# Performance work log

Hardware: AMD Instinct MI355X
Metric: run time of the kernel (lower is better)

Reference implementation:

```python
import jax, jax.numpy as jnp
import numpy as np
from jax import lax

BN_EPS = 1e-5
SP_NEAR = 2


def fps(xyz, m):
    # xyz: [b, n, c] -> indices [b, m]; deterministic start at index 0
    b, n, _ = xyz.shape
    def step(carry, _):
        dist, far = carry
        centroid = jnp.take_along_axis(xyz, far[:, None, None], axis=1)  # [b,1,c]
        d = jnp.sum((xyz - centroid) ** 2, axis=-1)                      # [b,n]
        dist = jnp.minimum(dist, d)
        return (dist, jnp.argmax(dist, axis=-1).astype(jnp.int32)), far
    init = (jnp.full((b, n), jnp.inf, xyz.dtype), jnp.zeros((b,), jnp.int32))
    _, idxs = lax.scan(step, init, None, length=m)
    return jnp.transpose(idxs)  # [b, m]


def knn(x, k):
    # x: [b, n, c] -> k nearest (incl. self) indices [b, n, k]
    sq = jnp.sum(x * x, axis=-1)
    d = sq[:, :, None] + sq[:, None, :] - 2.0 * jnp.einsum('bnc,bmc->bnm', x, x)
    return lax.top_k(-d, k)[1]


def gather_cf(x, idx):
    # channel-first index_points: x [b, c, n], idx [b, ...] -> [b, c, *idx.shape[1:]]
    b, c = x.shape[:2]
    flat = idx.reshape(b, -1)
    g = jnp.take_along_axis(x, flat[:, None, :], axis=2)
    return g.reshape((b, c) + idx.shape[1:])


def gather_cl(x, idx):
    # channel-last index_points: x [b, n, c], idx [b, ...] -> [b, *idx.shape[1:], c]
    b, c = x.shape[0], x.shape[-1]
    flat = idx.reshape(b, -1)
    g = jnp.take_along_axis(x, flat[:, :, None], axis=1)
    return g.reshape((b,) + idx.shape[1:] + (c,))


def bn_act(x, gamma, beta, nd):
    # inference-mode BatchNorm (running mean 0, var 1) + exact GELU; Dropout is identity in eval
    shp = (1, -1) + (1,) * nd
    scale = 1.0 / jnp.sqrt(1.0 + BN_EPS)
    return jax.nn.gelu(gamma.reshape(shp) * (x * scale) + beta.reshape(shp), approximate=False)


def setup_inputs() -> dict:
    key = jax.random.key(0)
    ks = jax.random.split(key, 8)
    BS, SP_IN, SP_OUT, DN_IN, DN_OUT = 128, 256, 256, 128, 128
    N_STK, N_STK_PNT, COOR = 32, 32, 32
    return {
        'sparse_fea': jax.random.normal(ks[0], (BS, SP_IN, N_STK), jnp.float32),
        'dense_fea': jax.random.normal(ks[1], (BS, DN_IN, N_STK, N_STK_PNT), jnp.float32),
        'stk_coor': jax.random.normal(ks[2], (BS, N_STK, COOR), jnp.float32),
        'n_stk_center': 16,
        'sp_w': jax.random.normal(ks[3], (SP_OUT, 2 * SP_IN), jnp.float32) * 0.02,
        'sp_b': jnp.zeros((SP_OUT,), jnp.float32),
        'sp_g': jnp.ones((SP_OUT,), jnp.float32),
        'sp_beta': jnp.zeros((SP_OUT,), jnp.float32),
        'dn_w': jax.random.normal(ks[4], (DN_OUT, 2 * DN_IN), jnp.float32) * 0.02,
        'dn_b': jnp.zeros((DN_OUT,), jnp.float32),
        'dn_g': jnp.ones((DN_OUT,), jnp.float32),
        'dn_beta': jnp.zeros((DN_OUT,), jnp.float32),
        'ds_w': jax.random.normal(ks[5], (DN_OUT, DN_IN, 1, 3), jnp.float32) * 0.05,
        'ds_b': jnp.zeros((DN_OUT,), jnp.float32),
        'ds_g': jnp.ones((DN_OUT,), jnp.float32),
        'ds_beta': jnp.zeros((DN_OUT,), jnp.float32),
    }


def reference(sparse_fea, dense_fea, stk_coor, n_stk_center,
              sp_w, sp_b, sp_g, sp_beta,
              dn_w, dn_b, dn_g, dn_beta,
              ds_w, ds_b, ds_g, ds_beta):
    bs, dn_in, n_stk, n_stk_pnt = dense_fea.shape
    fps_idx = fps(stk_coor, n_stk_center)            # [b, m]
    # --- sparse branch ---
    sc = gather_cf(sparse_fea, fps_idx)              # [b, c, m]
    knn_all = knn(stk_coor, SP_NEAR)                 # [b, n, k]
    knn_fps = gather_cl(knn_all, fps_idx)            # [b, m, k]
    sn = gather_cf(sparse_fea, knn_fps)              # [b, c, m, k]
    sa = sn - sc[:, :, :, None]
    sp_x = jnp.concatenate([sa, jnp.broadcast_to(sc[:, :, :, None], sa.shape)], axis=1)  # [b,2c,m,k]
    sp_x = jnp.einsum('bimk,oi->bomk', sp_x, sp_w) + sp_b[None, :, None, None]
    sp_x = bn_act(sp_x, sp_g, sp_beta, 2)
    sparse_out = jnp.max(sp_x, axis=3)               # [b, sp_out, m]
    # --- dense branch ---
    # 'b c s sp -> b s (sp c)'
    d_flat = jnp.transpose(dense_fea, (0, 2, 3, 1)).reshape(bs, n_stk, n_stk_pnt * dn_in)
    dc = gather_cl(d_flat, fps_idx)                  # [b, m, sp*c]
    dnb = gather_cl(d_flat, knn_fps)                 # [b, m, k, sp*c]
    da = dnb - dc[:, :, None, :]
    dcat = jnp.concatenate([da, jnp.broadcast_to(dc[:, :, None, :], da.shape)], axis=3)  # [b,m,k,2*sp*c]
    # 'b s n (sp c) -> b c s sp n' with sp=n_stk_pnt (exact torch reshape semantics)
    d5 = dcat.reshape(bs, fps_idx.shape[1], SP_NEAR, n_stk_pnt, 2 * dn_in)
    d5 = jnp.transpose(d5, (0, 4, 1, 3, 2))          # [b, 2c, m, sp, k]
    d5 = jnp.einsum('bimpn,oi->bompn', d5, dn_w) + dn_b[None, :, None, None, None]
    d5 = bn_act(d5, dn_g, dn_beta, 3)
    d4 = jnp.max(d5, axis=4)                         # [b, dn_out, m, sp]
    y = lax.conv_general_dilated(d4, ds_w, window_strides=(1, 2), padding=((0, 0), (1, 1)),
                                 dimension_numbers=('NCHW', 'OIHW', 'NCHW')) + ds_b[None, :, None, None]
    dense_out = bn_act(y, ds_g, ds_beta, 2)          # [b, dn_out, m, sp//2]
    coor_out = gather_cl(stk_coor, fps_idx)          # [b, m, coor]
    return sparse_out, dense_out, coor_out
```

## Files before the change

### kernel.cpp

```cpp
#include <hip/hip_runtime.h>


typedef unsigned short u16;
typedef unsigned int   u32;
typedef __attribute__((ext_vector_type(8))) short bf16x8;
typedef __attribute__((ext_vector_type(4))) float f32x4;

#define BN_SCALE 0.9999950000374997f

__device__ __forceinline__ float gelu_f(float x){
  return 0.5f*x*(1.0f + erff(x*0.70710678118654752f));
}
__device__ __forceinline__ u16 f2bf(float f){
  u32 x = __float_as_uint(f);
  x += 0x7fffu + ((x>>16)&1u);
  return (u16)(x>>16);
}

__global__ __launch_bounds__(256) void k_prep(
    const float* __restrict__ dn_w, const float* __restrict__ ds_w, const float* __restrict__ sp_w,
    const float* __restrict__ coor,
    u16* __restrict__ wdb, u16* __restrict__ wcb, u16* __restrict__ wsb,
    int* __restrict__ fps_idx, int* __restrict__ nn_idx, float* __restrict__ coor_out)
{
  int blk = blockIdx.x, t = threadIdx.x;
  if (blk < 128){
    int w = blk*256 + t;
    int j=w&7, lane=(w>>3)&63, tile=w>>9;
    int kt=tile>>3, ot=tile&7;
    int o=ot*16+(lane&15), i=kt*32+((lane>>4)&3)*8+j;
    wdb[w] = f2bf(dn_w[o*256+i]);
  } else if (blk < 320){
    int w = (blk-128)*256 + t;
    int j=w&7, lane=(w>>3)&63, tile=w>>9;
    int kt=tile>>3, ot=tile&7;
    int o=ot*16+(lane&15), k=kt*32+((lane>>4)&3)*8+j;
    wcb[w] = f2bf(ds_w[o*384+k]);
  } else if (blk < 832){
    int w = (blk-320)*256 + t;
    int j=w&7, lane=(w>>3)&63, tile=w>>9;
    int kt=tile>>4, ot=tile&15;
    int o=ot*16+(lane&15), i=kt*32+((lane>>4)&3)*8+j;
    wsb[w] = f2bf(sp_w[o*512+i]);
  } else {
    int b = blk - 832;
    __shared__ float Xs[32*33];
    __shared__ float D[32*33];
    __shared__ int   s_sel[16];
    for (int i=t;i<1024;i+=256) Xs[(i>>5)*33 + (i&31)] = coor[b*1024+i];
    __syncthreads();
    #pragma unroll
    for (int k2=0;k2<4;k2++){
      int p=t+k2*256, i=p>>5, j=p&31;
      float d=0.f;
      #pragma unroll
      for (int c=0;c<32;c++){ float df=Xs[i*33+c]-Xs[j*33+c]; d+=df*df; }
      D[i*33+j]=d;
    }
    __syncthreads();
    if (t < 64){
      int j = t & 31;
      float dist = 3.0e38f;
      int far = 0;
      #pragma unroll
      for (int it=0; it<16; ++it){
        if (t==0) s_sel[it]=far;
        dist = fminf(dist, D[far*33+j]);
        float v=dist; int idx=j;
        #pragma unroll
        for (int off=16; off>=1; off>>=1){
          float v2=__shfl_xor(v,off,32); int i2=__shfl_xor(idx,off,32);
          if (v2>v || (v2==v && i2<idx)){ v=v2; idx=i2; }
        }
        far = idx;
      }
      if (t==0){
        #pragma unroll
        for (int it=0;it<16;++it) fps_idx[b*16+it]=s_sel[it];
      }
    }
    __syncthreads();
    {
      int wv=t>>6, j=t&31;
      #pragma unroll
      for (int q=0;q<4;q++){
        int it = wv*4+q, sel = s_sel[it];
        float d = D[sel*33+j];
        if (j==sel) d=3.0e38f;
        float v=d; int idx=j;
        #pragma unroll
        for (int off=16; off>=1; off>>=1){
          float v2=__shfl_xor(v,off,32); int i2=__shfl_xor(idx,off,32);
          if (v2<v || (v2==v && i2<idx)){ v=v2; idx=i2; }
        }
        if ((t&63)==0) nn_idx[b*16+it]=idx;
      }
    }
    for (int q=t;q<512;q+=256){
      int mm=q>>5, c=q&31;
      coor_out[b*512+q] = Xs[s_sel[mm]*33 + c];
    }
  }
}

__global__ __launch_bounds__(256) void k_main(
    const float* __restrict__ sfea, const u16* __restrict__ wsb,
    const float* __restrict__ sp_b, const float* __restrict__ sp_g, const float* __restrict__ sp_be,
    const float* __restrict__ dfea, const u16* __restrict__ wdb,
    const float* __restrict__ dn_b, const float* __restrict__ dn_g, const float* __restrict__ dn_be,
    const u16* __restrict__ wcb,
    const float* __restrict__ ds_b, const float* __restrict__ ds_g, const float* __restrict__ ds_be,
    const int* __restrict__ fps_idx, const int* __restrict__ nn_idx,
    float* __restrict__ out_sp, float* __restrict__ out_dn)
{
  __shared__ char smem[36352];
  __shared__ int SI[64];
  int blk=blockIdx.x;
  int t=threadIdx.x, lane=t&63, wv=t>>6, quad=lane>>4, col=lane&15;
  if (blk < 64){
    int b0 = blk*2;
    u16*   Xb = (u16*)smem;
    float* P  = (float*)(smem+33280);
    if (t<64){
      int bb=t>>5, q=t&31, b=b0+bb;
      SI[t] = ((q<16) ? fps_idx[b*16+q] : nn_idx[b*16+(q-16)]) & 31;
    }
    { float A = sp_g[t]*BN_SCALE; P[t]=A; P[256+t]=fmaf(sp_b[t],A,sp_be[t]); }
    __syncthreads();
    #pragma unroll
    for (int bb=0;bb<2;bb++){
      const float* row = sfea + (b0+bb)*8192 + t*32;
      #pragma unroll
      for (int m=0;m<16;m++){
        float vc=row[SI[bb*32+m]], vn=row[SI[bb*32+16+m]];
        Xb[bb*8320 + m*520 + t]       = f2bf(vn-vc);
        Xb[bb*8320 + m*520 + 256 + t] = f2bf(vc);
      }
    }
    __syncthreads();
    #pragma unroll
    for (int oh=0;oh<2;oh++){
      f32x4 accA[2][2]={}, accB[2][2]={};
      #pragma unroll
      for (int kt=0;kt<16;kt++){
        bf16x8 bf0 = *(const bf16x8*)&Xb[        col*520 + kt*32 + quad*8];
        bf16x8 bf1 = *(const bf16x8*)&Xb[8320 +  col*520 + kt*32 + quad*8];
        #pragma unroll
        for (int r=0;r<2;r++){
          bf16x8 afr = *(const bf16x8*)&wsb[((kt*16 + oh*8 + wv + r*4)*64+lane)*8];
          if (kt<8){
            accA[0][r]=__builtin_amdgcn_mfma_f32_16x16x32_bf16(afr,bf0,accA[0][r],0,0,0);
            accA[1][r]=__builtin_amdgcn_mfma_f32_16x16x32_bf16(afr,bf1,accA[1][r],0,0,0);
          } else {
            accB[0][r]=__builtin_amdgcn_mfma_f32_16x16x32_bf16(afr,bf0,accB[0][r],0,0,0);
            accB[1][r]=__builtin_amdgcn_mfma_f32_16x16x32_bf16(afr,bf1,accB[1][r],0,0,0);
          }
        }
      }
      #pragma unroll
      for (int bb=0;bb<2;bb++){
        #pragma unroll
        for (int r=0;r<2;r++){
          #pragma unroll
          for (int reg=0;reg<4;reg++){
            int o = oh*128 + (wv+r*4)*16 + quad*4 + reg;
            float A=P[o], Bv=P[256+o];
            float k1 = accA[bb][r][reg]+accB[bb][r][reg];
            float k0 = accB[bb][r][reg];
            float v = fmaxf(gelu_f(fmaf(k1,A,Bv)), gelu_f(fmaf(k0,A,Bv)));
            out_sp[((b0+bb)*256+o)*16 + col] = v;
          }
        }
      }
    }
  } else {
    int d=blk-64;
    int b = ((d>>6)<<3) | (d&7), m0 = ((d>>3)&7)*2;
    u16* Vb = (u16*)smem;
    u16* Bc = (u16*)smem;
    float* Pd = (float*)(smem+33792);
    if (t < 128){
      float A  = dn_g[t]*BN_SCALE; float Bv = fmaf(dn_b[t], A, dn_be[t]);
      float Ac = ds_g[t]*BN_SCALE; float Cv = fmaf(ds_b[t], Ac, ds_be[t]);
      Pd[t]=A; Pd[128+t]=Bv; Pd[256+t]=Ac; Pd[384+t]=Cv;
      Pd[512+t]=gelu_f(Bv);
    }
    int ci0=fps_idx[b*16+m0]&31,   ni0=nn_idx[b*16+m0]&31;
    int ci1=fps_idx[b*16+m0+1]&31, ni1=nn_idx[b*16+m0+1]&31;
    const float* Db = dfea + b*131072;
    #pragma unroll
    for (int it=0; it<4; it++){
      int w = t + it*256;
      int mi = w>>9, q = w&511;
      int cp = q>>3, xq = q&7;
      int c = cp*2, x = xq*4;
      int ci = mi ? ci1 : ci0, ni = mi ? ni1 : ni0;
      const float* base = Db + c*1024 + x;
      float4 fcA = *(const float4*)(base + ci*32);
      float4 fnA = *(const float4*)(base + ni*32);
      float4 fcB = *(const float4*)(base + 1024 + ci*32);
      float4 fnB = *(const float4*)(base + 1024 + ni*32);
      u16* VbM = Vb + mi*8448;
      #pragma unroll
      for (int e=0;e<4;e++){
        int xx=x+e, dp=xx&1, p=xx>>1;
        u32 dlo = f2bf(((const float*)&fnA)[e] - ((const float*)&fcA)[e]);
        u32 dhi = f2bf(((const float*)&fnB)[e] - ((const float*)&fcB)[e]);
        u32 clo = f2bf(((const float*)&fcA)[e]);
        u32 chi = f2bf(((const float*)&fcB)[e]);
        *(u32*)&VbM[p*264 + dp*128 + c]      = dlo | (dhi<<16);
        *(u32*)&VbM[(16+p)*264 + dp*128 + c] = clo | (chi<<16);
      }
    }
    bf16x8 af0[2];
    #pragma unroll
    for (int r=0;r<2;r++) af0[r] = *(const bf16x8*)&wdb[((wv + r*4)*64+lane)*8];
    __syncthreads();
    f32x4 acc[2][4]={};
    #pragma unroll
    for (int kt=0;kt<8;kt++){
      bf16x8 bfr[4];
      #pragma unroll
      for (int mi=0;mi<2;mi++)
        #pragma unroll
        for (int pt=0;pt<2;pt++)
          bfr[mi*2+pt] = *(const bf16x8*)&Vb[mi*8448 + (pt*16+col)*264 + kt*32 + quad*8];
      #pragma unroll
      for (int r=0;r<2;r++){
        bf16x8 afr = (kt==0) ? af0[r] : *(const bf16x8*)&wdb[((kt*8+wv+r*4)*64+lane)*8];
        #pragma unroll
        for (int q=0;q<4;q++)
          acc[r][q]=__builtin_amdgcn_mfma_f32_16x16x32_bf16(afr,bfr[q],acc[r][q],0,0,0);
      }
    }
    __syncthreads();
    { int mi=t>>7, o=t&127; Bc[mi*6272 + o*3] = 0; }
    #pragma unroll
    for (int r=0;r<2;r++){
      #pragma unroll
      for (int mi=0;mi<2;mi++){
        u16* BcM = Bc + mi*6272;
        #pragma unroll
        for (int pt=0;pt<2;pt++){
          #pragma unroll
          for (int reg=0;reg<4;reg++){
            int o = (wv+r*4)*16 + quad*4 + reg;
            int p = pt*16 + col;
            float val = gelu_f(fmaf(acc[r][mi*2+pt][reg], Pd[o], Pd[128+o]));
            if (pt==0) val = fmaxf(val, Pd[512+o]);
            u16 bv = f2bf(val);
            if (p&1){
              BcM[((p-1)>>1)*392 + o*3 + 2] = bv;
              if (p<31) BcM[((p+1)>>1)*392 + o*3 + 0] = bv;
            } else {
              BcM[(p>>1)*392 + o*3 + 1] = bv;
            }
          }
        }
      }
    }
    __syncthreads();
    f32x4 cacc[2][2]={};
    #pragma unroll
    for (int kt=0;kt<12;kt++){
      bf16x8 cb0 = *(const bf16x8*)&Bc[       col*392 + kt*32 + quad*8];
      bf16x8 cb1 = *(const bf16x8*)&Bc[6272 + col*392 + kt*32 + quad*8];
      #pragma unroll
      for (int r=0;r<2;r++){
        bf16x8 afr = *(const bf16x8*)&wcb[((kt*8+wv+r*4)*64+lane)*8];
        cacc[r][0]=__builtin_amdgcn_mfma_f32_16x16x32_bf16(afr,cb0,cacc[r][0],0,0,0);
        cacc[r][1]=__builtin_amdgcn_mfma_f32_16x16x32_bf16(afr,cb1,cacc[r][1],0,0,0);
      }
    }
    #pragma unroll
    for (int r=0;r<2;r++){
      #pragma unroll
      for (int mi=0;mi<2;mi++){
        #pragma unroll
        for (int reg=0;reg<4;reg++){
          int o = (wv+r*4)*16 + quad*4 + reg;
          float val = gelu_f(fmaf(cacc[r][mi][reg], Pd[256+o], Pd[384+o]));
          out_dn[(b*128+o)*256 + (m0+mi)*16 + col] = val;
        }
      }
    }
  }
}

extern "C" void kernel_launch(void* const* d_in, const int* in_sizes, int n_in,
                              void* d_out, int out_size, void* d_ws, size_t ws_size,
                              hipStream_t stream) {
  const float* sparse_fea = (const float*)d_in[0];
  const float* dense_fea  = (const float*)d_in[1];
  const float* stk_coor   = (const float*)d_in[2];
  const float* sp_w  = (const float*)d_in[4];
  const float* sp_b  = (const float*)d_in[5];
  const float* sp_g  = (const float*)d_in[6];
  const float* sp_be = (const float*)d_in[7];
  const float* dn_w  = (const float*)d_in[8];
  const float* dn_b  = (const float*)d_in[9];
  const float* dn_g  = (const float*)d_in[10];
  const float* dn_be = (const float*)d_in[11];
  const float* ds_w  = (const float*)d_in[12];
  const float* ds_b  = (const float*)d_in[13];
  const float* ds_g  = (const float*)d_in[14];
  const float* ds_be = (const float*)d_in[15];

  float* out = (float*)d_out;
  int* fps_idx = (int*)d_ws;
  int* nn_idx  = fps_idx + 2048;
  u16* wdb = (u16*)((char*)d_ws + 16384);
  u16* wcb = (u16*)((char*)d_ws + 81920);
  u16* wsb = (u16*)((char*)d_ws + 180224);

  k_prep<<<960, 256, 0, stream>>>(dn_w, ds_w, sp_w, stk_coor,
                                  wdb, wcb, wsb, fps_idx, nn_idx, out + 4718592);
  k_main<<<1088, 256, 0, stream>>>(sparse_fea, wsb, sp_b, sp_g, sp_be,
                                   dense_fea, wdb, dn_b, dn_g, dn_be,
                                   wcb, ds_b, ds_g, ds_be,
                                   fps_idx, nn_idx, out, out + 524288);
}
```

Before: 168.1 us.

## Halve per-block work in k_main to double grid size and occupancy

```diff
diff --git a/kernel.cpp b/kernel.cpp
--- a/kernel.cpp
+++ b/kernel.cpp
@@ -103,7 +103,7 @@
   }
 }
 
-__global__ __launch_bounds__(256) void k_main(
+__global__ __launch_bounds__(256,6) void k_main(
     const float* __restrict__ sfea, const u16* __restrict__ wsb,
     const float* __restrict__ sp_b, const float* __restrict__ sp_g, const float* __restrict__ sp_be,
     const float* __restrict__ dfea, const u16* __restrict__ wdb,
@@ -113,94 +113,79 @@
     const int* __restrict__ fps_idx, const int* __restrict__ nn_idx,
     float* __restrict__ out_sp, float* __restrict__ out_dn)
 {
-  __shared__ char smem[36352];
-  __shared__ int SI[64];
+  __shared__ char smem[19456];
+  __shared__ int SI[32];
   int blk=blockIdx.x;
   int t=threadIdx.x, lane=t&63, wv=t>>6, quad=lane>>4, col=lane&15;
-  if (blk < 64){
-    int b0 = blk*2;
+  if (blk < 128){
+    int b = blk;
     u16*   Xb = (u16*)smem;
-    float* P  = (float*)(smem+33280);
-    if (t<64){
-      int bb=t>>5, q=t&31, b=b0+bb;
-      SI[t] = ((q<16) ? fps_idx[b*16+q] : nn_idx[b*16+(q-16)]) & 31;
+    float* P  = (float*)(smem+16640);
+    if (t<32){
+      SI[t] = ((t<16) ? fps_idx[b*16+t] : nn_idx[b*16+(t-16)]) & 31;
     }
     { float A = sp_g[t]*BN_SCALE; P[t]=A; P[256+t]=fmaf(sp_b[t],A,sp_be[t]); }
     __syncthreads();
-    #pragma unroll
-    for (int bb=0;bb<2;bb++){
-      const float* row = sfea + (b0+bb)*8192 + t*32;
+    {
+      const float* row = sfea + b*8192 + t*32;
       #pragma unroll
       for (int m=0;m<16;m++){
-        float vc=row[SI[bb*32+m]], vn=row[SI[bb*32+16+m]];
-        Xb[bb*8320 + m*520 + t]       = f2bf(vn-vc);
-        Xb[bb*8320 + m*520 + 256 + t] = f2bf(vc);
+        float vc=row[SI[m]], vn=row[SI[16+m]];
+        Xb[m*520 + t]       = f2bf(vn-vc);
+        Xb[m*520 + 256 + t] = f2bf(vc);
       }
     }
     __syncthreads();
     #pragma unroll
     for (int oh=0;oh<2;oh++){
-      f32x4 accA[2][2]={}, accB[2][2]={};
+      f32x4 accA[2]={}, accB[2]={};
       #pragma unroll
       for (int kt=0;kt<16;kt++){
-        bf16x8 bf0 = *(const bf16x8*)&Xb[        col*520 + kt*32 + quad*8];
-        bf16x8 bf1 = *(const bf16x8*)&Xb[8320 +  col*520 + kt*32 + quad*8];
+        bf16x8 bf0 = *(const bf16x8*)&Xb[col*520 + kt*32 + quad*8];
         #pragma unroll
         for (int r=0;r<2;r++){
           bf16x8 afr = *(const bf16x8*)&wsb[((kt*16 + oh*8 + wv + r*4)*64+lane)*8];
-          if (kt<8){
-            accA[0][r]=__builtin_amdgcn_mfma_f32_16x16x32_bf16(afr,bf0,accA[0][r],0,0,0);
-            accA[1][r]=__builtin_amdgcn_mfma_f32_16x16x32_bf16(afr,bf1,accA[1][r],0,0,0);
-          } else {
-            accB[0][r]=__builtin_amdgcn_mfma_f32_16x16x32_bf16(afr,bf0,accB[0][r],0,0,0);
-            accB[1][r]=__builtin_amdgcn_mfma_f32_16x16x32_bf16(afr,bf1,accB[1][r],0,0,0);
-          }
-        }
-      }
-      #pragma unroll
-      for (int bb=0;bb<2;bb++){
-        #pragma unroll
-        for (int r=0;r<2;r++){
-          #pragma unroll
-          for (int reg=0;reg<4;reg++){
-            int o = oh*128 + (wv+r*4)*16 + quad*4 + reg;
-            float A=P[o], Bv=P[256+o];
-            float k1 = accA[bb][r][reg]+accB[bb][r][reg];
-            float k0 = accB[bb][r][reg];
-            float v = fmaxf(gelu_f(fmaf(k1,A,Bv)), gelu_f(fmaf(k0,A,Bv)));
-            out_sp[((b0+bb)*256+o)*16 + col] = v;
-          }
+          if (kt<8) accA[r]=__builtin_amdgcn_mfma_f32_16x16x32_bf16(afr,bf0,accA[r],0,0,0);
+          else      accB[r]=__builtin_amdgcn_mfma_f32_16x16x32_bf16(afr,bf0,accB[r],0,0,0);
+        }
+      }
+      #pragma unroll
+      for (int r=0;r<2;r++){
+        #pragma unroll
+        for (int reg=0;reg<4;reg++){
+          int o = oh*128 + (wv+r*4)*16 + quad*4 + reg;
+          float A=P[o], Bv=P[256+o];
+          float k1 = accA[r][reg]+accB[r][reg];
+          float k0 = accB[r][reg];
+          float v = fmaxf(gelu_f(fmaf(k1,A,Bv)), gelu_f(fmaf(k0,A,Bv)));
+          out_sp[(b*256+o)*16 + col] = v;
         }
       }
     }
   } else {
-    int d=blk-64;
-    int b = ((d>>6)<<3) | (d&7), m0 = ((d>>3)&7)*2;
+    int d=blk-128;
+    int b = ((d>>7)<<3) | (d&7), m = (d>>3)&15;
     u16* Vb = (u16*)smem;
     u16* Bc = (u16*)smem;
-    float* Pd = (float*)(smem+33792);
+    float* Pd = (float*)(smem+16896);
     if (t < 128){
       float A  = dn_g[t]*BN_SCALE; float Bv = fmaf(dn_b[t], A, dn_be[t]);
       float Ac = ds_g[t]*BN_SCALE; float Cv = fmaf(ds_b[t], Ac, ds_be[t]);
       Pd[t]=A; Pd[128+t]=Bv; Pd[256+t]=Ac; Pd[384+t]=Cv;
       Pd[512+t]=gelu_f(Bv);
     }
-    int ci0=fps_idx[b*16+m0]&31,   ni0=nn_idx[b*16+m0]&31;
-    int ci1=fps_idx[b*16+m0+1]&31, ni1=nn_idx[b*16+m0+1]&31;
+    int ci=fps_idx[b*16+m]&31, ni=nn_idx[b*16+m]&31;
     const float* Db = dfea + b*131072;
     #pragma unroll
-    for (int it=0; it<4; it++){
+    for (int it=0; it<2; it++){
       int w = t + it*256;
-      int mi = w>>9, q = w&511;
-      int cp = q>>3, xq = q&7;
+      int cp = w>>3, xq = w&7;
       int c = cp*2, x = xq*4;
-      int ci = mi ? ci1 : ci0, ni = mi ? ni1 : ni0;
       const float* base = Db + c*1024 + x;
       float4 fcA = *(const float4*)(base + ci*32);
       float4 fnA = *(const float4*)(base + ni*32);
       float4 fcB = *(const float4*)(base + 1024 + ci*32);
       float4 fnB = *(const float4*)(base + 1024 + ni*32);
-      u16* VbM = Vb + mi*8448;
       #pragma unroll
       for (int e=0;e<4;e++){
         int xx=x+e, dp=xx&1, p=xx>>1;
@@ -208,80 +193,69 @@
         u32 dhi = f2bf(((const float*)&fnB)[e] - ((const float*)&fcB)[e]);
         u32 clo = f2bf(((const float*)&fcA)[e]);
         u32 chi = f2bf(((const float*)&fcB)[e]);
-        *(u32*)&VbM[p*264 + dp*128 + c]      = dlo | (dhi<<16);
-        *(u32*)&VbM[(16+p)*264 + dp*128 + c] = clo | (chi<<16);
+        *(u32*)&Vb[p*264 + dp*128 + c]      = dlo | (dhi<<16);
+        *(u32*)&Vb[(16+p)*264 + dp*128 + c] = clo | (chi<<16);
       }
     }
     bf16x8 af0[2];
     #pragma unroll
     for (int r=0;r<2;r++) af0[r] = *(const bf16x8*)&wdb[((wv + r*4)*64+lane)*8];
     __syncthreads();
-    f32x4 acc[2][4]={};
+    f32x4 acc[2][2]={};
     #pragma unroll
     for (int kt=0;kt<8;kt++){
-      bf16x8 bfr[4];
-      #pragma unroll
-      for (int mi=0;mi<2;mi++)
-        #pragma unroll
-        for (int pt=0;pt<2;pt++)
-          bfr[mi*2+pt] = *(const bf16x8*)&Vb[mi*8448 + (pt*16+col)*264 + kt*32 + quad*8];
+      bf16x8 bfr[2];
+      #pragma unroll
+      for (int pt=0;pt<2;pt++)
+        bfr[pt] = *(const bf16x8*)&Vb[(pt*16+col)*264 + kt*32 + quad*8];
       #pragma unroll
       for (int r=0;r<2;r++){
         bf16x8 afr = (kt==0) ? af0[r] : *(const bf16x8*)&wdb[((kt*8+wv+r*4)*64+lane)*8];
         #pragma unroll
-        for (int q=0;q<4;q++)
-          acc[r][q]=__builtin_amdgcn_mfma_f32_16x16x32_bf16(afr,bfr[q],acc[r][q],0,0,0);
-      }
-    }
-    __syncthreads();
-    { int mi=t>>7, o=t&127; Bc[mi*6272 + o*3] = 0; }
+        for (int pt=0;pt<2;pt++)
+          acc[r][pt]=__builtin_amdgcn_mfma_f32_16x16x32_bf16(afr,bfr[pt],acc[r][pt],0,0,0);
+      }
+    }
+    __syncthreads();
+    if (t<128) Bc[t*3] = 0;
     #pragma unroll
     for (int r=0;r<2;r++){
       #pragma unroll
-      for (int mi=0;mi<2;mi++){
-        u16* BcM = Bc + mi*6272;
-        #pragma unroll
-        for (int pt=0;pt<2;pt++){
-          #pragma unroll
-          for (int reg=0;reg<4;reg++){
-            int o = (wv+r*4)*16 + quad*4 + reg;
-            int p = pt*16 + col;
-            float val = gelu_f(fmaf(acc[r][mi*2+pt][reg], Pd[o], Pd[128+o]));
-            if (pt==0) val = fmaxf(val, Pd[512+o]);
-            u16 bv = f2bf(val);
-            if (p&1){
-              BcM[((p-1)>>1)*392 + o*3 + 2] = bv;
-              if (p<31) BcM[((p+1)>>1)*392 + o*3 + 0] = bv;
-            } else {
-              BcM[(p>>1)*392 + o*3 + 1] = bv;
-            }
+      for (int pt=0;pt<2;pt++){
+        #pragma unroll
+        for (int reg=0;reg<4;reg++){
+          int o = (wv+r*4)*16 + quad*4 + reg;
+          int p = pt*16 + col;
+          float val = gelu_f(fmaf(acc[r][pt][reg], Pd[o], Pd[128+o]));
+          if (pt==0) val = fmaxf(val, Pd[512+o]);
+          u16 bv = f2bf(val);
+          if (p&1){
+            Bc[((p-1)>>1)*392 + o*3 + 2] = bv;
+            if (p<31) Bc[((p+1)>>1)*392 + o*3 + 0] = bv;
+          } else {
+            Bc[(p>>1)*392 + o*3 + 1] = bv;
           }
         }
       }
     }
     __syncthreads();
-    f32x4 cacc[2][2]={};
+    f32x4 cacc[2]={};
     #pragma unroll
     for (int kt=0;kt<12;kt++){
-      bf16x8 cb0 = *(const bf16x8*)&Bc[       col*392 + kt*32 + quad*8];
-      bf16x8 cb1 = *(const bf16x8*)&Bc[6272 + col*392 + kt*32 + quad*8];
+      bf16x8 cb0 = *(const bf16x8*)&Bc[col*392 + kt*32 + quad*8];
       #pragma unroll
       for (int r=0;r<2;r++){
         bf16x8 afr = *(const bf16x8*)&wcb[((kt*8+wv+r*4)*64+lane)*8];
-        cacc[r][0]=__builtin_amdgcn_mfma_f32_16x16x32_bf16(afr,cb0,cacc[r][0],0,0,0);
-        cacc[r][1]=__builtin_amdgcn_mfma_f32_16x16x32_bf16(afr,cb1,cacc[r][1],0,0,0);
+        cacc[r]=__builtin_amdgcn_mfma_f32_16x16x32_bf16(afr,cb0,cacc[r],0,0,0);
       }
     }
     #pragma unroll
     for (int r=0;r<2;r++){
       #pragma unroll
-      for (int mi=0;mi<2;mi++){
-        #pragma unroll
-        for (int reg=0;reg<4;reg++){
-          int o = (wv+r*4)*16 + quad*4 + reg;
-          float val = gelu_f(fmaf(cacc[r][mi][reg], Pd[256+o], Pd[384+o]));
-          out_dn[(b*128+o)*256 + (m0+mi)*16 + col] = val;
-        }
+      for (int reg=0;reg<4;reg++){
+        int o = (wv+r*4)*16 + quad*4 + reg;
+        float val = gelu_f(fmaf(cacc[r][reg], Pd[256+o], Pd[384+o]));
+        out_dn[(b*128+o)*256 + m*16 + col] = val;
       }
     }
   }
@@ -315,7 +289,7 @@
 
   k_prep<<<960, 256, 0, stream>>>(dn_w, ds_w, sp_w, stk_coor,
                                   wdb, wcb, wsb, fps_idx, nn_idx, out + 4718592);
-  k_main<<<1088, 256, 0, stream>>>(sparse_fea, wsb, sp_b, sp_g, sp_be,
+  k_main<<<2176, 256, 0, stream>>>(sparse_fea, wsb, sp_b, sp_g, sp_be,
                                    dense_fea, wdb, dn_b, dn_g, dn_be,
                                    wcb, ds_b, ds_g, ds_be,
                                    fps_idx, nn_idx, out, out + 524288);
```

Result: no change. 166.8 us (-0.8%).
